# Kernel tuning notes

Hardware: AMD Instinct MI355X
Metric: run time of the kernel (lower is better)

## Reference

```python
import jax, jax.numpy as jnp
import numpy as np

N, D, K, G = 262144, 256, 1024, 4
C = D // G
BETA = 0.5


def setup_inputs() -> dict:
    key = jax.random.key(0)
    k1, k2 = jax.random.split(key)
    z = jax.random.normal(k1, (N, D), dtype=jnp.float32)
    # original init: uniform(-1/K, 1/K)
    codebooks = jax.random.uniform(k2, (G, K, C), dtype=jnp.float32,
                                   minval=-1.0 / K, maxval=1.0 / K)
    return {"z": z, "codebooks": codebooks}


def reference(z, codebooks):
    # z: [N, D] -> [N, G, C]; codebooks: [G, K, C]
    zg = z.reshape(-1, G, C)
    # squared distances: ||z||^2 + ||e||^2 - 2 z.e  -> [N, G, K]
    z_sq = jnp.sum(zg ** 2, axis=-1, keepdims=True)            # [N, G, 1]
    e_sq = jnp.sum(codebooks ** 2, axis=-1)                    # [G, K]
    dots = jnp.einsum('ngc,gkc->ngk', zg, codebooks)           # [N, G, K]
    d = z_sq + e_sq[None, :, :] - 2.0 * dots
    idx = jnp.argmin(d, axis=-1)                               # [N, G]
    # gather codes: [N, G, C]
    zq = codebooks[jnp.arange(G)[None, :], idx]
    # per-group VQ loss, averaged over groups (means over N and C per group)
    sg = jax.lax.stop_gradient
    commit = jnp.mean((sg(zq) - zg) ** 2, axis=(0, 2))         # [G]
    embed = jnp.mean((zq - sg(zg)) ** 2, axis=(0, 2))          # [G]
    loss = jnp.mean(BETA * commit + embed)
    # straight-through estimator
    zq_st = zg + sg(zq - zg)
    return zq_st.reshape(-1, D), loss
```

## Files before the change

### kernel.cpp

```cpp
#include <hip/hip_runtime.h>
#include <stdint.h>

typedef int   i32x4 __attribute__((ext_vector_type(4)));
typedef int   i32x8 __attribute__((ext_vector_type(8)));
typedef float f32x16 __attribute__((ext_vector_type(16)));

#define NTOK 262144
#define DDIM 256
#define KCB  1024
#define GG   4
#define CC   64
#define WAVES 4
#define ROWS_PER_BLK (WAVES * 64)
#define NBLKX (NTOK / ROWS_PER_BLK)
#define NPART (NBLKX * GG)
#define CB8B  (KCB * CC)

static __device__ __forceinline__ uint32_t umin32(uint32_t a, uint32_t b) { return a < b ? a : b; }

typedef __attribute__((address_space(1))) const void gv_t;
typedef __attribute__((address_space(3))) void lv_t;
static __device__ __forceinline__ void gl_lds16(const void* g, void* l) {
    __builtin_amdgcn_global_load_lds((gv_t*)g, (lv_t*)l, 16, 0, 0);
}
static __device__ __forceinline__ void gl_lds4(const void* g, void* l) {
    __builtin_amdgcn_global_load_lds((gv_t*)g, (lv_t*)l, 4, 0, 0);
}

__global__ __launch_bounds__(64) void vq_prep(const float* __restrict__ cb,
                                              unsigned short* __restrict__ cb8,
                                              float* __restrict__ esq05) {
    int gk = blockIdx.x;
    int c  = threadIdx.x;
    float v = cb[(size_t)gk * CC + c];
    float s = v * v;
    #pragma unroll
    for (int off = 32; off; off >>= 1) s += __shfl_down(s, off, 64);
    if (c == 0) esq05[gk] = 0.5f + s;
    if (c < 32) {
        float v0 = cb[(size_t)gk * CC + 2 * c]     * 1024.0f;
        float v1 = cb[(size_t)gk * CC + 2 * c + 1] * 1024.0f;
        int p = __builtin_amdgcn_cvt_pk_fp8_f32(v0, v1, 0, false);
        cb8[gk * 32 + c] = (unsigned short)(p & 0xFFFF);
    }
}

__global__ __launch_bounds__(256, 2) void vq_argmin(const float* __restrict__ z,
                                                    const unsigned char* __restrict__ cb8,
                                                    const float* __restrict__ esq05,
                                                    unsigned short* __restrict__ idx,
                                                    float* __restrict__ part) {
    const int tid  = threadIdx.x;
    const int lane = tid & 63;
    const int w    = tid >> 6;
    const int g    = blockIdx.y;
    const int r0   = blockIdx.x * ROWS_PER_BLK + w * 64;
    const int c5   = lane & 31;
    const int h    = lane >> 5;

    __shared__ __align__(16) char sb[CB8B + KCB * 4];
    __shared__ float ls[WAVES];

    const unsigned char* cbg8 = cb8 + (size_t)g * CB8B;
    const float*         eg   = esq05 + (size_t)g * KCB;

    #pragma unroll
    for (int j = 0; j < 16; ++j) {
        int i = w + 4 * j;
        int s = i >> 1, slot = i & 1;
        const unsigned char* src = cbg8 + ((s * 32 + c5) * CC + h * 32 + slot * 16);
        gl_lds16(src, &sb[i * 1024]);
    }
    #pragma unroll
    for (int p = 0; p < 4; ++p)
        gl_lds4(eg + p * 256 + tid, &sb[CB8B + p * 1024 + w * 256]);

    i32x8 a[2];
    float zsq[2];
    #pragma unroll
    for (int f = 0; f < 2; ++f) {
        const float* zp = z + (size_t)(r0 + f * 32 + c5) * DDIM + g * CC + h * 32;
        int w8[8];
        float s = 0.0f;
        #pragma unroll
        for (int j = 0; j < 8; ++j) {
            float4 v = ((const float4*)zp)[j];
            s += v.x * v.x + v.y * v.y + v.z * v.z + v.w * v.w;
            int p = __builtin_amdgcn_cvt_pk_fp8_f32(-2.0f * v.x, -2.0f * v.y, 0, false);
            p     = __builtin_amdgcn_cvt_pk_fp8_f32(-2.0f * v.z, -2.0f * v.w, p, true);
            w8[j] = p;
        }
        a[f] = (i32x8){w8[0], w8[1], w8[2], w8[3], w8[4], w8[5], w8[6], w8[7]};
        s += __shfl_xor(s, 32, 64);
        zsq[f] = s;
    }

    uint32_t run[2][16];
    #pragma unroll
    for (int f = 0; f < 2; ++f)
        #pragma unroll
        for (int r = 0; r < 16; ++r) run[f][r] = 0xFFFFFFFFu;

    __syncthreads();

    const float* eb = (const float*)(sb + CB8B);

    #pragma unroll 1
    for (int s2 = 0; s2 < 32; s2 += 2) {
        const char* p0 = sb + (size_t)s2 * 2048;
        i32x4 aLo = *(const i32x4*)(p0 + lane * 16);
        i32x4 aHi = *(const i32x4*)(p0 + 1024 + lane * 16);
        i32x4 bLo = *(const i32x4*)(p0 + 2048 + lane * 16);
        i32x4 bHi = *(const i32x4*)(p0 + 3072 + lane * 16);
        i32x8 bA = (i32x8){aLo[0], aLo[1], aLo[2], aLo[3], aHi[0], aHi[1], aHi[2], aHi[3]};
        i32x8 bB = (i32x8){bLo[0], bLo[1], bLo[2], bLo[3], bHi[0], bHi[1], bHi[2], bHi[3]};
        float eA = eb[s2 * 32 + c5];
        float eB = eb[s2 * 32 + 32 + c5];
        f32x16 ceA, ceB;
        #pragma unroll
        for (int i = 0; i < 16; ++i) { ceA[i] = eA; ceB[i] = eB; }
        uint32_t codeA = (uint32_t)(s2 * 32 + c5);

        __builtin_amdgcn_s_setprio(1);
        f32x16 acc00 = __builtin_amdgcn_mfma_scale_f32_32x32x64_f8f6f4(
            a[0], bA, ceA, 0, 0, 0, 0x7F7F7F7F, 0, 0x75757575);
        f32x16 acc01 = __builtin_amdgcn_mfma_scale_f32_32x32x64_f8f6f4(
            a[0], bB, ceB, 0, 0, 0, 0x7F7F7F7F, 0, 0x75757575);
        __builtin_amdgcn_s_setprio(0);
        #pragma unroll
        for (int r = 0; r < 16; ++r) {
            uint32_t kA = (__float_as_uint(acc00[r]) & 0xFFFFFC00u) | codeA;
            uint32_t kB = (__float_as_uint(acc01[r]) & 0xFFFFFC00u) | (codeA + 32u);
            run[0][r] = umin32(run[0][r], umin32(kA, kB));
        }
        __builtin_amdgcn_s_setprio(1);
        f32x16 acc10 = __builtin_amdgcn_mfma_scale_f32_32x32x64_f8f6f4(
            a[1], bA, ceA, 0, 0, 0, 0x7F7F7F7F, 0, 0x75757575);
        f32x16 acc11 = __builtin_amdgcn_mfma_scale_f32_32x32x64_f8f6f4(
            a[1], bB, ceB, 0, 0, 0, 0x7F7F7F7F, 0, 0x75757575);
        __builtin_amdgcn_s_setprio(0);
        #pragma unroll
        for (int r = 0; r < 16; ++r) {
            uint32_t kA = (__float_as_uint(acc10[r]) & 0xFFFFFC00u) | codeA;
            uint32_t kB = (__float_as_uint(acc11[r]) & 0xFFFFFC00u) | (codeA + 32u);
            run[1][r] = umin32(run[1][r], umin32(kA, kB));
        }
    }

    float lsum = 0.0f;
    #pragma unroll
    for (int f = 0; f < 2; ++f) {
        #pragma unroll
        for (int r = 0; r < 16; ++r) {
            uint32_t k = run[f][r];
            k = umin32(k, __shfl_xor(k, 1, 64));
            k = umin32(k, __shfl_xor(k, 2, 64));
            k = umin32(k, __shfl_xor(k, 4, 64));
            k = umin32(k, __shfl_xor(k, 8, 64));
            k = umin32(k, __shfl_xor(k, 16, 64));
            int   kw     = (int)(k & 1023u);
            float minval = __uint_as_float(k & 0xFFFFFC00u) - 0.5f;
            int rloc = (r & 3) + 8 * (r >> 2) + 4 * h;
            int grow = r0 + f * 32 + rloc;
            float zs = __shfl(zsq[f], rloc, 64);
            if (c5 == 0) {
                idx[(grow << 2) | g] = (unsigned short)kw;
                lsum += zs + minval;
            }
        }
    }
    #pragma unroll
    for (int off = 32; off; off >>= 1) lsum += __shfl_down(lsum, off, 64);

    if (lane == 0) ls[w] = lsum;
    __syncthreads();
    if (tid == 0) {
        float s = 0.0f;
        #pragma unroll
        for (int i = 0; i < WAVES; ++i) s += ls[i];
        part[blockIdx.y * NBLKX + blockIdx.x] = s;
    }
}

__global__ __launch_bounds__(256) void vq_gather(const unsigned short* __restrict__ idx,
                                                 const float* __restrict__ cb32,
                                                 float* __restrict__ out) {
    const int stride = gridDim.x * 256;
    const int total  = NTOK * (DDIM / 4);
    for (int i = blockIdx.x * 256 + threadIdx.x; i < total; i += stride) {
        int row = i >> 6;
        int d4  = i & 63;
        int g   = d4 >> 4;
        int c4  = d4 & 15;
        int k   = idx[(row << 2) | g];
        float4 v = *(const float4*)(cb32 + (size_t)(((g << 10) + k) << 6) + (c4 << 2));
        *(float4*)(out + ((size_t)row << 8) + (d4 << 2)) = v;
    }
}

__global__ __launch_bounds__(256) void vq_final(const float* __restrict__ part,
                                                float* __restrict__ out_loss) {
    __shared__ float ls[4];
    float s = 0.0f;
    for (int i = threadIdx.x; i < NPART; i += 256) s += part[i];
    #pragma unroll
    for (int off = 32; off; off >>= 1) s += __shfl_down(s, off, 64);
    int lane = threadIdx.x & 63, w = threadIdx.x >> 6;
    if (lane == 0) ls[w] = s;
    __syncthreads();
    if (threadIdx.x == 0) {
        *out_loss = 1.5f * (ls[0] + ls[1] + ls[2] + ls[3]) * (1.0f / ((float)NTOK * (float)DDIM));
    }
}

extern "C" void kernel_launch(void* const* d_in, const int* in_sizes, int n_in,
                              void* d_out, int out_size, void* d_ws, size_t ws_size,
                              hipStream_t stream) {
    const float* z  = (const float*)d_in[0];
    const float* cb = (const float*)d_in[1];
    float* out = (float*)d_out;

    char* ws = (char*)d_ws;
    unsigned short* cb8 = (unsigned short*)ws;
    float* esq05 = (float*)(ws + 256 * 1024);
    float* part  = (float*)(ws + 256 * 1024 + 16 * 1024);
    unsigned short* idx = (unsigned short*)(ws + 256 * 1024 + 32 * 1024);

    vq_prep<<<GG * KCB, 64, 0, stream>>>(cb, cb8, esq05);

    dim3 grid(NBLKX, GG);
    vq_argmin<<<grid, 256, 0, stream>>>(z, (const unsigned char*)cb8, esq05, idx, part);

    vq_gather<<<4096, 256, 0, stream>>>(idx, cb, out);

    vq_final<<<1, 256, 0, stream>>>(part, out + (size_t)NTOK * DDIM);
}
```

Measured before the change: 239.7 us.

## Process four row fragments per wave and prefetch codebook tiles from LDS

Each wave now handles 128 rows (four 32-row fragments) instead of 64, so every codebook B-fragment read from LDS feeds twice as many MFMAs. The next iteration's codebook fragments are loaded into registers before the current MFMAs issue, overlapping LDS latency with compute, and the s_setprio hints are removed. Register pressure rises (more A operands and 64 running-min registers), which may lower occupancy under the 2-blocks launch bound, and the grid has half as many blocks.

```diff
diff --git a/kernel.cpp b/kernel.cpp
--- a/kernel.cpp
+++ b/kernel.cpp
@@ -11,7 +11,8 @@
 #define GG   4
 #define CC   64
 #define WAVES 4
-#define ROWS_PER_BLK (WAVES * 64)
+#define FRW  4
+#define ROWS_PER_BLK (WAVES * FRW * 32)
 #define NBLKX (NTOK / ROWS_PER_BLK)
 #define NPART (NBLKX * GG)
 #define CB8B  (KCB * CC)
@@ -54,7 +55,7 @@
     const int lane = tid & 63;
     const int w    = tid >> 6;
     const int g    = blockIdx.y;
-    const int r0   = blockIdx.x * ROWS_PER_BLK + w * 64;
+    const int r0   = blockIdx.x * ROWS_PER_BLK + w * (FRW * 32);
     const int c5   = lane & 31;
     const int h    = lane >> 5;
 
@@ -75,10 +76,10 @@
     for (int p = 0; p < 4; ++p)
         gl_lds4(eg + p * 256 + tid, &sb[CB8B + p * 1024 + w * 256]);
 
-    i32x8 a[2];
-    float zsq[2];
-    #pragma unroll
-    for (int f = 0; f < 2; ++f) {
+    i32x8 a[FRW];
+    float zsq[FRW];
+    #pragma unroll
+    for (int f = 0; f < FRW; ++f) {
         const float* zp = z + (size_t)(r0 + f * 32 + c5) * DDIM + g * CC + h * 32;
         int w8[8];
         float s = 0.0f;
@@ -95,9 +96,9 @@
         zsq[f] = s;
     }
 
-    uint32_t run[2][16];
-    #pragma unroll
-    for (int f = 0; f < 2; ++f)
+    uint32_t run[FRW][16];
+    #pragma unroll
+    for (int f = 0; f < FRW; ++f)
         #pragma unroll
         for (int r = 0; r < 16; ++r) run[f][r] = 0xFFFFFFFFu;
 
@@ -105,15 +106,24 @@
 
     const float* eb = (const float*)(sb + CB8B);
 
+    i32x4 c0, c1, c2, c3;
+    {
+        c0 = *(const i32x4*)(sb + lane * 16);
+        c1 = *(const i32x4*)(sb + 1024 + lane * 16);
+        c2 = *(const i32x4*)(sb + 2048 + lane * 16);
+        c3 = *(const i32x4*)(sb + 3072 + lane * 16);
+    }
     #pragma unroll 1
     for (int s2 = 0; s2 < 32; s2 += 2) {
-        const char* p0 = sb + (size_t)s2 * 2048;
-        i32x4 aLo = *(const i32x4*)(p0 + lane * 16);
-        i32x4 aHi = *(const i32x4*)(p0 + 1024 + lane * 16);
-        i32x4 bLo = *(const i32x4*)(p0 + 2048 + lane * 16);
-        i32x4 bHi = *(const i32x4*)(p0 + 3072 + lane * 16);
-        i32x8 bA = (i32x8){aLo[0], aLo[1], aLo[2], aLo[3], aHi[0], aHi[1], aHi[2], aHi[3]};
-        i32x8 bB = (i32x8){bLo[0], bLo[1], bLo[2], bLo[3], bHi[0], bHi[1], bHi[2], bHi[3]};
+        int ns = (s2 + 2) & 31;
+        const char* pn = sb + (size_t)ns * 2048;
+        i32x4 n0 = *(const i32x4*)(pn + lane * 16);
+        i32x4 n1 = *(const i32x4*)(pn + 1024 + lane * 16);
+        i32x4 n2 = *(const i32x4*)(pn + 2048 + lane * 16);
+        i32x4 n3 = *(const i32x4*)(pn + 3072 + lane * 16);
+
+        i32x8 bA = (i32x8){c0[0], c0[1], c0[2], c0[3], c1[0], c1[1], c1[2], c1[3]};
+        i32x8 bB = (i32x8){c2[0], c2[1], c2[2], c2[3], c3[0], c3[1], c3[2], c3[3]};
         float eA = eb[s2 * 32 + c5];
         float eB = eb[s2 * 32 + 32 + c5];
         f32x16 ceA, ceB;
@@ -121,35 +131,25 @@
         for (int i = 0; i < 16; ++i) { ceA[i] = eA; ceB[i] = eB; }
         uint32_t codeA = (uint32_t)(s2 * 32 + c5);
 
-        __builtin_amdgcn_s_setprio(1);
-        f32x16 acc00 = __builtin_amdgcn_mfma_scale_f32_32x32x64_f8f6f4(
-            a[0], bA, ceA, 0, 0, 0, 0x7F7F7F7F, 0, 0x75757575);
-        f32x16 acc01 = __builtin_amdgcn_mfma_scale_f32_32x32x64_f8f6f4(
-            a[0], bB, ceB, 0, 0, 0, 0x7F7F7F7F, 0, 0x75757575);
-        __builtin_amdgcn_s_setprio(0);
-        #pragma unroll
-        for (int r = 0; r < 16; ++r) {
-            uint32_t kA = (__float_as_uint(acc00[r]) & 0xFFFFFC00u) | codeA;
-            uint32_t kB = (__float_as_uint(acc01[r]) & 0xFFFFFC00u) | (codeA + 32u);
-            run[0][r] = umin32(run[0][r], umin32(kA, kB));
+        #pragma unroll
+        for (int f = 0; f < FRW; ++f) {
+            f32x16 accA = __builtin_amdgcn_mfma_scale_f32_32x32x64_f8f6f4(
+                a[f], bA, ceA, 0, 0, 0, 0x7F7F7F7F, 0, 0x75757575);
+            f32x16 accB = __builtin_amdgcn_mfma_scale_f32_32x32x64_f8f6f4(
+                a[f], bB, ceB, 0, 0, 0, 0x7F7F7F7F, 0, 0x75757575);
+            #pragma unroll
+            for (int r = 0; r < 16; ++r) {
+                uint32_t kA = (__float_as_uint(accA[r]) & 0xFFFFFC00u) | codeA;
+                uint32_t kB = (__float_as_uint(accB[r]) & 0xFFFFFC00u) | (codeA + 32u);
+                run[f][r] = umin32(run[f][r], umin32(kA, kB));
+            }
         }
-        __builtin_amdgcn_s_setprio(1);
-        f32x16 acc10 = __builtin_amdgcn_mfma_scale_f32_32x32x64_f8f6f4(
-            a[1], bA, ceA, 0, 0, 0, 0x7F7F7F7F, 0, 0x75757575);
-        f32x16 acc11 = __builtin_amdgcn_mfma_scale_f32_32x32x64_f8f6f4(
-            a[1], bB, ceB, 0, 0, 0, 0x7F7F7F7F, 0, 0x75757575);
-        __builtin_amdgcn_s_setprio(0);
-        #pragma unroll
-        for (int r = 0; r < 16; ++r) {
-            uint32_t kA = (__float_as_uint(acc10[r]) & 0xFFFFFC00u) | codeA;
-            uint32_t kB = (__float_as_uint(acc11[r]) & 0xFFFFFC00u) | (codeA + 32u);
-            run[1][r] = umin32(run[1][r], umin32(kA, kB));
-        }
+        c0 = n0; c1 = n1; c2 = n2; c3 = n3;
     }
 
     float lsum = 0.0f;
     #pragma unroll
-    for (int f = 0; f < 2; ++f) {
+    for (int f = 0; f < FRW; ++f) {
         #pragma unroll
         for (int r = 0; r < 16; ++r) {
             uint32_t k = run[f][r];
```

Result: no change. 237.8 us (-0.8%).
